# Kernel tuning notes

Hardware: AMD Instinct MI355X
Metric: run time of the kernel (lower is better)

The kernel has to match this reference:

```python
import jax, jax.numpy as jnp
import numpy as np

N_NODES = 50000


def gcn_conv(x, src, dst, W, b, n_nodes):
    """PyG-style GCNConv: x' = D^-1/2 (A + I) D^-1/2 (x W) + b.
    src/dst already include self-loops."""
    h = x @ W  # [N, C_out]
    # symmetric normalization from degree (with self-loops, unit edge weight)
    deg = jax.ops.segment_sum(jnp.ones_like(dst, dtype=h.dtype), dst,
                              num_segments=n_nodes)  # [N]
    dinv = jnp.where(deg > 0, jax.lax.rsqrt(deg), 0.0)
    norm = dinv[src] * dinv[dst]  # [E]
    msg = h[src] * norm[:, None]  # gather + scale, [E, C_out]
    out = jax.ops.segment_sum(msg, dst, num_segments=n_nodes)  # scatter-add
    return out + b


def setup_inputs() -> dict:
    key = jax.random.key(0)
    k1, k2, k3, k4, k5, k6 = jax.random.split(key, 6)
    in_c, hid_c, out_c = 128, 64, 64
    x = jax.random.normal(k1, (N_NODES, in_c), dtype=jnp.float32)
    edge_index = jax.random.randint(k2, (2, 800000), 0, N_NODES, dtype=jnp.int64)
    # Glorot-ish init for weights, zeros for bias (as PyG default)
    W1 = jax.random.normal(k3, (in_c, hid_c), dtype=jnp.float32) / np.sqrt(in_c)
    b1 = jnp.zeros((hid_c,), dtype=jnp.float32)
    W2 = jax.random.normal(k4, (hid_c, out_c), dtype=jnp.float32) / np.sqrt(hid_c)
    b2 = jnp.zeros((out_c,), dtype=jnp.float32)
    return {"x": x, "edge_index": edge_index, "W1": W1, "b1": b1,
            "W2": W2, "b2": b2}


def reference(x, edge_index, W1, b1, W2, b2):
    n = x.shape[0]
    loops = jnp.arange(n, dtype=edge_index.dtype)
    src = jnp.concatenate([edge_index[0], loops])  # add self-loops
    dst = jnp.concatenate([edge_index[1], loops])
    h = gcn_conv(x, src, dst, W1, b1, n)
    h = jax.nn.relu(h)
    return gcn_conv(h, src, dst, W2, b2, n)
```

## Files before the change

kernel.cpp:

```cpp
#include <hip/hip_runtime.h>
#include <hip/hip_fp16.h>


#define C_HID 64

static inline size_t alignup(size_t x) { return (x + 255) & ~(size_t)255; }

typedef __attribute__((address_space(3))) unsigned int lds_uint;
typedef __attribute__((address_space(1))) const unsigned int glob_uint;

__device__ __forceinline__ int blockScanIncl256(int v, int* wsum) {
    const int lane = threadIdx.x & 63, wav = threadIdx.x >> 6;
    int s = v;
#pragma unroll
    for (int off = 1; off < 64; off <<= 1) {
        int t = __shfl_up(s, off);
        if (lane >= off) s += t;
    }
    if (lane == 63) wsum[wav] = s;
    __syncthreads();
    if (wav == 0 && lane < 4) {
        int ws = wsum[lane];
#pragma unroll
        for (int off = 1; off < 4; off <<= 1) {
            int t = __shfl_up(ws, off);
            if (lane >= off) ws += t;
        }
        wsum[lane] = ws;
    }
    __syncthreads();
    return (wav ? wsum[wav - 1] : 0) + s;
}

__device__ __forceinline__ void gridbar(int* bar, int k, int nblk) {
    __syncthreads();
    if (threadIdx.x == 0) {
        __threadfence();
        __hip_atomic_fetch_add(&bar[k], 1, __ATOMIC_RELEASE, __HIP_MEMORY_SCOPE_AGENT);
        while (__hip_atomic_load(&bar[k], __ATOMIC_RELAXED, __HIP_MEMORY_SCOPE_AGENT) < nblk)
            __builtin_amdgcn_s_sleep(2);
        __threadfence();
    }
    __syncthreads();
}

template <int K>
__global__ __launch_bounds__(256) void gemm1_hist_kernel(
    const float* __restrict__ X, const float* __restrict__ W,
    const int* __restrict__ dst, __half* __restrict__ outh,
    int* __restrict__ S, int* __restrict__ bar,
    int n, int E, int ePer, int nb) {
    constexpr int KP = K + 4;
    __shared__ float Xs[64 * KP];
    __shared__ float Ws[K * 64];
    __shared__ int h[256];
    const int t = threadIdx.x;
    const int lane = t & 63;
    const int wav = t >> 6;

    if ((int)blockIdx.x < nb) {
        if (blockIdx.x == 0 && t < 8) bar[t] = 0;
        h[t] = 0;
        __syncthreads();
        int beg = blockIdx.x * ePer, end = min(E, beg + ePer);
        for (int e = beg + t; e < end; e += 256)
            atomicAdd(&h[dst[e] >> 8], 1);
        __syncthreads();
        for (int b = t; b < nb; b += 256)
            S[(size_t)b * nb + blockIdx.x] = h[b];
        return;
    }

    const int row0 = ((int)blockIdx.x - nb) * 64;
    {
        const char* gb = (const char*)W;
        char* lb = (char*)Ws;
        for (int off = wav * 1024; off < K * 64 * 4; off += 4096)
            __builtin_amdgcn_global_load_lds((glob_uint*)(gb + off + lane * 16),
                                             (lds_uint*)(lb + off), 16, 0, 0);
    }
    if (row0 + 64 <= n) {
        const float4* g4 = (const float4*)(X + (size_t)row0 * K);
        for (int i = t; i < 64 * (K / 4); i += 256) {
            float4 v = g4[i];
            int r = i / (K / 4), k0 = (i % (K / 4)) * 4;
            *(float4*)&Xs[r * KP + k0] = v;
        }
    } else {
        for (int i = t; i < 64 * K; i += 256) {
            int r = i / K, k = i % K;
            Xs[r * KP + k] = (row0 + r < n) ? X[(size_t)(row0 + r) * K + k] : 0.0f;
        }
    }
    __syncthreads();

    const int tx = t & 15;
    const int ty = t >> 4;
    float acc[4][4] = {{0.f}};
#pragma unroll 2
    for (int k0 = 0; k0 < K; k0 += 4) {
        float4 a0 = *(const float4*)&Xs[(4 * ty + 0) * KP + k0];
        float4 a1 = *(const float4*)&Xs[(4 * ty + 1) * KP + k0];
        float4 a2 = *(const float4*)&Xs[(4 * ty + 2) * KP + k0];
        float4 a3 = *(const float4*)&Xs[(4 * ty + 3) * KP + k0];
        float4 b0 = *(const float4*)&Ws[(k0 + 0) * 64 + 4 * tx];
        float4 b1 = *(const float4*)&Ws[(k0 + 1) * 64 + 4 * tx];
        float4 b2 = *(const float4*)&Ws[(k0 + 2) * 64 + 4 * tx];
        float4 b3 = *(const float4*)&Ws[(k0 + 3) * 64 + 4 * tx];
        const float* ap[4] = {(const float*)&a0, (const float*)&a1,
                              (const float*)&a2, (const float*)&a3};
        const float* bp[4] = {(const float*)&b0, (const float*)&b1,
                              (const float*)&b2, (const float*)&b3};
#pragma unroll
        for (int r = 0; r < 4; ++r)
#pragma unroll
            for (int kk = 0; kk < 4; ++kk) {
                float av = ap[r][kk];
#pragma unroll
                for (int c = 0; c < 4; ++c)
                    acc[r][c] = fmaf(av, bp[kk][c], acc[r][c]);
            }
    }
#pragma unroll
    for (int r = 0; r < 4; ++r) {
        int row = row0 + 4 * ty + r;
        if (row < n) {
            __half2 p01 = __floats2half2_rn(acc[r][0], acc[r][1]);
            __half2 p23 = __floats2half2_rn(acc[r][2], acc[r][3]);
            float2 st;
            ((__half2*)&st)[0] = p01;
            ((__half2*)&st)[1] = p23;
            *(float2*)&outh[(size_t)row * 64 + 4 * tx] = st;
        }
    }
}

__global__ __launch_bounds__(256) void csr_kernel(
    const int* __restrict__ src, const int* __restrict__ dst, int E, int ePer,
    int* __restrict__ S, int* __restrict__ T, int* __restrict__ bar,
    unsigned* __restrict__ ebuf, int* __restrict__ row_ptr,
    float* __restrict__ dinv, int* __restrict__ esrc, int n, int nb) {
    __shared__ int arr[256];
    __shared__ int texcl[256];
    __shared__ int wsum[4];
    const int b = blockIdx.x;
    const int t = threadIdx.x;

    {
        int v = (t < nb) ? S[(size_t)b * nb + t] : 0;
        int incl = blockScanIncl256(v, wsum);
        if (t < nb) S[(size_t)b * nb + t] = incl - v;
        if (t == 0) T[b] = wsum[3];
    }
    gridbar(bar, 0, nb);

    {
        int v = (t < nb) ? T[t] : 0;
        int incl = blockScanIncl256(v, wsum);
        texcl[t] = incl - v;
    }
    __syncthreads();

    if (t < nb) arr[t] = S[(size_t)t * nb + b] + texcl[t];
    __syncthreads();
    {
        int beg = b * ePer, end = min(E, beg + ePer);
        for (int e = beg + t; e < end; e += 256) {
            int d = dst[e];
            int s = src[e];
            int pos = atomicAdd(&arr[d >> 8], 1);
            ebuf[pos] = ((unsigned)s << 8) | (unsigned)(d & 255);
        }
    }
    gridbar(bar, 1, nb);

    const int node0 = b << 8;
    const int ebeg = texcl[b];
    const int eend = (b + 1 < nb) ? texcl[b + 1] : E;
    arr[t] = 0;
    __syncthreads();
    for (int e = ebeg + t; e < eend; e += 256)
        atomicAdd(&arr[ebuf[e] & 255], 1);
    __syncthreads();
    int deg = arr[t];
    int incl = blockScanIncl256(deg, wsum);
    int excl = incl - deg;
    __syncthreads();
    arr[t] = ebeg + excl;
    int v = node0 + t;
    if (v < n) {
        row_ptr[v + 1] = ebeg + incl;
        dinv[v] = rsqrtf(1.0f + (float)deg);
        if (v == 0) row_ptr[0] = 0;
    }
    __syncthreads();
    for (int e = ebeg + t; e < eend; e += 256) {
        unsigned p = ebuf[e];
        int pos = atomicAdd(&arr[p & 255], 1);
        esrc[pos] = (int)(p >> 8);
    }
}

__global__ __launch_bounds__(256) void agg1_gemm2_kernel(
    const __half* __restrict__ g1, const int* __restrict__ row_ptr,
    const int* __restrict__ esrc, const float* __restrict__ dinv,
    const float* __restrict__ b1, const float* __restrict__ W2,
    __half* __restrict__ g2, int n) {
    __shared__ float Bt[64][68];
    __shared__ float Ws2[64 * 64];
    const int t = threadIdx.x, lane = t & 63, wav = t >> 6;

    {
        const char* gb = (const char*)W2;
        char* lb = (char*)Ws2;
        for (int off = wav * 1024; off < 64 * 64 * 4; off += 4096)
            __builtin_amdgcn_global_load_lds((glob_uint*)(gb + off + lane * 16),
                                             (lds_uint*)(lb + off), 16, 0, 0);
    }

    const int g = t >> 2;
    const int c = t & 3;
    const int row0 = blockIdx.x * 64;
    const int v = row0 + g;
    const float4* __restrict__ hs4 = (const float4*)g1;

    if (v < n) {
        float acc[16];
        float dv0 = dinv[v];
        {
            size_t rb = (size_t)v * 8 + 2 * c;
            float4 r0 = hs4[rb], r1 = hs4[rb + 1];
            const __half2* h0 = (const __half2*)&r0;
            const __half2* h1 = (const __half2*)&r1;
#pragma unroll
            for (int q = 0; q < 4; ++q) {
                float2 f0 = __half22float2(h0[q]);
                float2 f1 = __half22float2(h1[q]);
                acc[2 * q] = f0.x * dv0;     acc[2 * q + 1] = f0.y * dv0;
                acc[8 + 2 * q] = f1.x * dv0; acc[9 + 2 * q] = f1.y * dv0;
            }
        }
        const int beg = row_ptr[v], end = row_ptr[v + 1];
        int j = beg;
        for (; j + 2 <= end; j += 2) {
            int s0 = esrc[j], s1 = esrc[j + 1];
            float d0 = dinv[s0], d1 = dinv[s1];
            size_t rb0 = (size_t)s0 * 8 + 2 * c, rb1 = (size_t)s1 * 8 + 2 * c;
            float4 a0 = hs4[rb0], a1 = hs4[rb0 + 1];
            float4 e0 = hs4[rb1], e1 = hs4[rb1 + 1];
            const __half2* pa0 = (const __half2*)&a0;
            const __half2* pa1 = (const __half2*)&a1;
            const __half2* pe0 = (const __half2*)&e0;
            const __half2* pe1 = (const __half2*)&e1;
#pragma unroll
            for (int q = 0; q < 4; ++q) {
                float2 f;
                f = __half22float2(pa0[q]);
                acc[2 * q] = fmaf(f.x, d0, acc[2 * q]);
                acc[2 * q + 1] = fmaf(f.y, d0, acc[2 * q + 1]);
                f = __half22float2(pa1[q]);
                acc[8 + 2 * q] = fmaf(f.x, d0, acc[8 + 2 * q]);
                acc[9 + 2 * q] = fmaf(f.y, d0, acc[9 + 2 * q]);
                f = __half22float2(pe0[q]);
                acc[2 * q] = fmaf(f.x, d1, acc[2 * q]);
                acc[2 * q + 1] = fmaf(f.y, d1, acc[2 * q + 1]);
                f = __half22float2(pe1[q]);
                acc[8 + 2 * q] = fmaf(f.x, d1, acc[8 + 2 * q]);
                acc[9 + 2 * q] = fmaf(f.y, d1, acc[9 + 2 * q]);
            }
        }
        if (j < end) {
            int s0 = esrc[j];
            float d0 = dinv[s0];
            size_t rb0 = (size_t)s0 * 8 + 2 * c;
            float4 a0 = hs4[rb0], a1 = hs4[rb0 + 1];
            const __half2* pa0 = (const __half2*)&a0;
            const __half2* pa1 = (const __half2*)&a1;
#pragma unroll
            for (int q = 0; q < 4; ++q) {
                float2 f;
                f = __half22float2(pa0[q]);
                acc[2 * q] = fmaf(f.x, d0, acc[2 * q]);
                acc[2 * q + 1] = fmaf(f.y, d0, acc[2 * q + 1]);
                f = __half22float2(pa1[q]);
                acc[8 + 2 * q] = fmaf(f.x, d0, acc[8 + 2 * q]);
                acc[9 + 2 * q] = fmaf(f.y, d0, acc[9 + 2 * q]);
            }
        }
        const float* bb = b1 + c * 16;
#pragma unroll
        for (int u = 0; u < 4; ++u) {
            float4 w;
            w.x = fmaxf(fmaf(acc[4 * u + 0], dv0, bb[4 * u + 0]), 0.f);
            w.y = fmaxf(fmaf(acc[4 * u + 1], dv0, bb[4 * u + 1]), 0.f);
            w.z = fmaxf(fmaf(acc[4 * u + 2], dv0, bb[4 * u + 2]), 0.f);
            w.w = fmaxf(fmaf(acc[4 * u + 3], dv0, bb[4 * u + 3]), 0.f);
            *(float4*)&Bt[g][c * 16 + 4 * u] = w;
        }
    } else {
#pragma unroll
        for (int u = 0; u < 4; ++u)
            *(float4*)&Bt[g][c * 16 + 4 * u] = make_float4(0.f, 0.f, 0.f, 0.f);
    }
    __syncthreads();

    const int tx = t & 15;
    const int ty = t >> 4;
    float a2[4][4] = {{0.f}};
#pragma unroll 2
    for (int k0 = 0; k0 < 64; k0 += 4) {
        float4 x0 = *(const float4*)&Bt[4 * ty + 0][k0];
        float4 x1 = *(const float4*)&Bt[4 * ty + 1][k0];
        float4 x2 = *(const float4*)&Bt[4 * ty + 2][k0];
        float4 x3 = *(const float4*)&Bt[4 * ty + 3][k0];
        float4 w0 = *(const float4*)&Ws2[(k0 + 0) * 64 + 4 * tx];
        float4 w1 = *(const float4*)&Ws2[(k0 + 1) * 64 + 4 * tx];
        float4 w2 = *(const float4*)&Ws2[(k0 + 2) * 64 + 4 * tx];
        float4 w3 = *(const float4*)&Ws2[(k0 + 3) * 64 + 4 * tx];
        const float* xp[4] = {(const float*)&x0, (const float*)&x1,
                              (const float*)&x2, (const float*)&x3};
        const float* wp[4] = {(const float*)&w0, (const float*)&w1,
                              (const float*)&w2, (const float*)&w3};
#pragma unroll
        for (int r = 0; r < 4; ++r)
#pragma unroll
            for (int kk = 0; kk < 4; ++kk) {
                float av = xp[r][kk];
#pragma unroll
                for (int cc = 0; cc < 4; ++cc)
                    a2[r][cc] = fmaf(av, wp[kk][cc], a2[r][cc]);
            }
    }
#pragma unroll
    for (int r = 0; r < 4; ++r) {
        int row = row0 + 4 * ty + r;
        if (row < n) {
            float dv = dinv[row];
            __half2 p01 = __floats2half2_rn(a2[r][0] * dv, a2[r][1] * dv);
            __half2 p23 = __floats2half2_rn(a2[r][2] * dv, a2[r][3] * dv);
            float2 st;
            ((__half2*)&st)[0] = p01;
            ((__half2*)&st)[1] = p23;
            *(float2*)&g2[(size_t)row * 64 + 4 * tx] = st;
        }
    }
}

__global__ __launch_bounds__(256) void aggregate2_kernel(
    const __half* __restrict__ hs,
    const int* __restrict__ row_ptr,
    const int* __restrict__ esrc,
    const float* __restrict__ dinv,
    const float* __restrict__ bias,
    float* __restrict__ out, int n) {
    const int v = blockIdx.x * 32 + (threadIdx.x >> 3);
    if (v >= n) return;
    const int c8 = threadIdx.x & 7;
    const float4* __restrict__ hs4 = (const float4*)hs;

    const int beg = row_ptr[v];
    const int end = row_ptr[v + 1];

    float acc[8];
    {
        float4 raw = hs4[(size_t)v * 8 + c8];
        const __half2* hp = (const __half2*)&raw;
#pragma unroll
        for (int q = 0; q < 4; ++q) {
            float2 f = __half22float2(hp[q]);
            acc[2 * q] = f.x; acc[2 * q + 1] = f.y;
        }
    }

    int j = beg;
    for (; j + 4 <= end; j += 4) {
        int s0 = esrc[j], s1 = esrc[j + 1], s2 = esrc[j + 2], s3 = esrc[j + 3];
        float4 r0 = hs4[(size_t)s0 * 8 + c8];
        float4 r1 = hs4[(size_t)s1 * 8 + c8];
        float4 r2 = hs4[(size_t)s2 * 8 + c8];
        float4 r3 = hs4[(size_t)s3 * 8 + c8];
        const __half2* h0 = (const __half2*)&r0;
        const __half2* h1 = (const __half2*)&r1;
        const __half2* h2 = (const __half2*)&r2;
        const __half2* h3 = (const __half2*)&r3;
#pragma unroll
        for (int q = 0; q < 4; ++q) {
            float2 f0 = __half22float2(h0[q]);
            float2 f1 = __half22float2(h1[q]);
            float2 f2 = __half22float2(h2[q]);
            float2 f3 = __half22float2(h3[q]);
            acc[2 * q]     += (f0.x + f1.x) + (f2.x + f3.x);
            acc[2 * q + 1] += (f0.y + f1.y) + (f2.y + f3.y);
        }
    }
    for (; j < end; ++j) {
        int s0 = esrc[j];
        float4 r0 = hs4[(size_t)s0 * 8 + c8];
        const __half2* h0 = (const __half2*)&r0;
#pragma unroll
        for (int q = 0; q < 4; ++q) {
            float2 f0 = __half22float2(h0[q]);
            acc[2 * q] += f0.x;
            acc[2 * q + 1] += f0.y;
        }
    }

    float dv = dinv[v];
    float4 b0 = *(const float4*)(bias + c8 * 8);
    float4 b1v = *(const float4*)(bias + c8 * 8 + 4);
    float4 o0, o1;
    o0.x = fmaf(acc[0], dv, b0.x); o0.y = fmaf(acc[1], dv, b0.y);
    o0.z = fmaf(acc[2], dv, b0.z); o0.w = fmaf(acc[3], dv, b0.w);
    o1.x = fmaf(acc[4], dv, b1v.x); o1.y = fmaf(acc[5], dv, b1v.y);
    o1.z = fmaf(acc[6], dv, b1v.z); o1.w = fmaf(acc[7], dv, b1v.w);
    float4* op = (float4*)(out + (size_t)v * 64 + c8 * 8);
    op[0] = o0;
    op[1] = o1;
}

extern "C" void kernel_launch(void* const* d_in, const int* in_sizes, int n_in,
                              void* d_out, int out_size, void* d_ws, size_t ws_size,
                              hipStream_t stream) {
    const float* x  = (const float*)d_in[0];
    const int*   ei = (const int*)d_in[1];
    const float* W1 = (const float*)d_in[2];
    const float* b1 = (const float*)d_in[3];
    const float* W2 = (const float*)d_in[4];
    const float* b2 = (const float*)d_in[5];
    float* out = (float*)d_out;

    const int C_IN = 128;
    const int n = in_sizes[0] / C_IN;
    const int E = in_sizes[1] / 2;
    const int* src = ei;
    const int* dst = ei + E;

    const int nb = (n + 255) >> 8;
    const int ngb = (n + 63) / 64;
    const int ePer = (E + nb - 1) / nb;

    char* w = (char*)d_ws;
    float*    dinv    = (float*)w;    w += alignup((size_t)n * sizeof(float));
    __half*   g1      = (__half*)w;   w += alignup((size_t)n * C_HID * sizeof(__half));
    __half*   g2      = (__half*)w;   w += alignup((size_t)n * C_HID * sizeof(__half));
    int*      row_ptr = (int*)w;      w += alignup((size_t)(n + 1) * sizeof(int));
    int*      S       = (int*)w;      w += alignup(((size_t)nb * nb + nb) * sizeof(int));
    int*      T       = S + (size_t)nb * nb;
    int*      bar     = (int*)w;      w += alignup(64 * sizeof(int));
    unsigned* ebuf    = (unsigned*)w; w += alignup((size_t)E * sizeof(unsigned));
    int*      esrc    = (int*)w;

    gemm1_hist_kernel<128><<<nb + ngb, 256, 0, stream>>>(
        x, W1, dst, g1, S, bar, n, E, ePer, nb);

    csr_kernel<<<nb, 256, 0, stream>>>(
        src, dst, E, ePer, S, T, bar, ebuf, row_ptr, dinv, esrc, n, nb);

    agg1_gemm2_kernel<<<ngb, 256, 0, stream>>>(
        g1, row_ptr, esrc, dinv, b1, W2, g2, n);

    aggregate2_kernel<<<(n + 31) / 32, 256, 0, stream>>>(
        g2, row_ptr, esrc, dinv, b2, out, n);
}
```

Before: 192.3 us.

## Replace grid-barrier CSR kernel with separate scan, scatter and build kernels

Splits the single persistent CSR-construction kernel, which used two software grid barriers built on atomics and spin-waits, into four kernels: per-row scan, scan of block totals, edge scatter, and per-bucket row-pointer build. Kernel boundaries now provide the ordering, which removes the barrier spinning and the need to reset barrier counters. The cost is three extra kernel launches, and the tiny single-block scan kernel adds serial latency between stages.

```diff
diff --git a/kernel.cpp b/kernel.cpp
--- a/kernel.cpp
+++ b/kernel.cpp
@@ -30,26 +30,13 @@
     }
     __syncthreads();
     return (wav ? wsum[wav - 1] : 0) + s;
-}
-
-__device__ __forceinline__ void gridbar(int* bar, int k, int nblk) {
-    __syncthreads();
-    if (threadIdx.x == 0) {
-        __threadfence();
-        __hip_atomic_fetch_add(&bar[k], 1, __ATOMIC_RELEASE, __HIP_MEMORY_SCOPE_AGENT);
-        while (__hip_atomic_load(&bar[k], __ATOMIC_RELAXED, __HIP_MEMORY_SCOPE_AGENT) < nblk)
-            __builtin_amdgcn_s_sleep(2);
-        __threadfence();
-    }
-    __syncthreads();
 }
 
 template <int K>
 __global__ __launch_bounds__(256) void gemm1_hist_kernel(
     const float* __restrict__ X, const float* __restrict__ W,
     const int* __restrict__ dst, __half* __restrict__ outh,
-    int* __restrict__ S, int* __restrict__ bar,
-    int n, int E, int ePer, int nb) {
+    int* __restrict__ S, int n, int E, int ePer, int nb) {
     constexpr int KP = K + 4;
     __shared__ float Xs[64 * KP];
     __shared__ float Ws[K * 64];
@@ -59,7 +46,6 @@
     const int wav = t >> 6;
 
     if ((int)blockIdx.x < nb) {
-        if (blockIdx.x == 0 && t < 8) bar[t] = 0;
         h[t] = 0;
         __syncthreads();
         int beg = blockIdx.x * ePer, end = min(E, beg + ePer);
@@ -135,48 +121,53 @@
     }
 }
 
-__global__ __launch_bounds__(256) void csr_kernel(
+__global__ __launch_bounds__(256) void scan_rows_kernel(
+    int* __restrict__ S, int* __restrict__ T, int nb) {
+    __shared__ int wsum[4];
+    const int b = blockIdx.x, t = threadIdx.x;
+    int v = (t < nb) ? S[(size_t)b * nb + t] : 0;
+    int incl = blockScanIncl256(v, wsum);
+    if (t < nb) S[(size_t)b * nb + t] = incl - v;
+    if (t == 0) T[b] = wsum[3];
+}
+
+__global__ __launch_bounds__(256) void scan_T_kernel(int* __restrict__ T, int nb) {
+    __shared__ int wsum[4];
+    const int t = threadIdx.x;
+    int v = (t < nb) ? T[t] : 0;
+    int incl = blockScanIncl256(v, wsum);
+    if (t < nb) T[t] = incl - v;
+    if (t == nb - 1) T[nb] = incl;
+}
+
+__global__ __launch_bounds__(256) void scatter_kernel(
     const int* __restrict__ src, const int* __restrict__ dst, int E, int ePer,
-    int* __restrict__ S, int* __restrict__ T, int* __restrict__ bar,
-    unsigned* __restrict__ ebuf, int* __restrict__ row_ptr,
-    float* __restrict__ dinv, int* __restrict__ esrc, int n, int nb) {
+    const int* __restrict__ S, const int* __restrict__ T,
+    unsigned* __restrict__ ebuf, int nb) {
     __shared__ int arr[256];
-    __shared__ int texcl[256];
+    const int b = blockIdx.x, t = threadIdx.x;
+    if (t < nb) arr[t] = S[(size_t)t * nb + b] + T[t];
+    __syncthreads();
+    int beg = b * ePer, end = min(E, beg + ePer);
+    for (int e = beg + t; e < end; e += 256) {
+        int d = dst[e];
+        int s = src[e];
+        int pos = atomicAdd(&arr[d >> 8], 1);
+        ebuf[pos] = ((unsigned)s << 8) | (unsigned)(d & 255);
+    }
+}
+
+__global__ __launch_bounds__(256) void build_kernel(
+    const unsigned* __restrict__ ebuf, const int* __restrict__ T,
+    int* __restrict__ row_ptr, float* __restrict__ dinv,
+    int* __restrict__ esrc, int n, int nb) {
+    __shared__ int arr[256];
     __shared__ int wsum[4];
-    const int b = blockIdx.x;
-    const int t = threadIdx.x;
-
-    {
-        int v = (t < nb) ? S[(size_t)b * nb + t] : 0;
-        int incl = blockScanIncl256(v, wsum);
-        if (t < nb) S[(size_t)b * nb + t] = incl - v;
-        if (t == 0) T[b] = wsum[3];
-    }
-    gridbar(bar, 0, nb);
-
-    {
-        int v = (t < nb) ? T[t] : 0;
-        int incl = blockScanIncl256(v, wsum);
-        texcl[t] = incl - v;
-    }
-    __syncthreads();
-
-    if (t < nb) arr[t] = S[(size_t)t * nb + b] + texcl[t];
-    __syncthreads();
-    {
-        int beg = b * ePer, end = min(E, beg + ePer);
-        for (int e = beg + t; e < end; e += 256) {
-            int d = dst[e];
-            int s = src[e];
-            int pos = atomicAdd(&arr[d >> 8], 1);
-            ebuf[pos] = ((unsigned)s << 8) | (unsigned)(d & 255);
-        }
-    }
-    gridbar(bar, 1, nb);
-
+    const int b = blockIdx.x, t = threadIdx.x;
     const int node0 = b << 8;
-    const int ebeg = texcl[b];
-    const int eend = (b + 1 < nb) ? texcl[b + 1] : E;
+    const int ebeg = T[b];
+    const int eend = T[b + 1];
+
     arr[t] = 0;
     __syncthreads();
     for (int e = ebeg + t; e < eend; e += 256)
@@ -444,17 +435,18 @@
     __half*   g1      = (__half*)w;   w += alignup((size_t)n * C_HID * sizeof(__half));
     __half*   g2      = (__half*)w;   w += alignup((size_t)n * C_HID * sizeof(__half));
     int*      row_ptr = (int*)w;      w += alignup((size_t)(n + 1) * sizeof(int));
-    int*      S       = (int*)w;      w += alignup(((size_t)nb * nb + nb) * sizeof(int));
-    int*      T       = S + (size_t)nb * nb;
-    int*      bar     = (int*)w;      w += alignup(64 * sizeof(int));
+    int*      S       = (int*)w;      w += alignup((size_t)nb * nb * sizeof(int));
+    int*      T       = (int*)w;      w += alignup((size_t)(nb + 1) * sizeof(int));
     unsigned* ebuf    = (unsigned*)w; w += alignup((size_t)E * sizeof(unsigned));
     int*      esrc    = (int*)w;
 
     gemm1_hist_kernel<128><<<nb + ngb, 256, 0, stream>>>(
-        x, W1, dst, g1, S, bar, n, E, ePer, nb);
-
-    csr_kernel<<<nb, 256, 0, stream>>>(
-        src, dst, E, ePer, S, T, bar, ebuf, row_ptr, dinv, esrc, n, nb);
+        x, W1, dst, g1, S, n, E, ePer, nb);
+
+    scan_rows_kernel<<<nb, 256, 0, stream>>>(S, T, nb);
+    scan_T_kernel<<<1, 256, 0, stream>>>(T, nb);
+    scatter_kernel<<<nb, 256, 0, stream>>>(src, dst, E, ePer, S, T, ebuf, nb);
+    build_kernel<<<nb, 256, 0, stream>>>(ebuf, T, row_ptr, dinv, esrc, n, nb);
 
     agg1_gemm2_kernel<<<ngb, 256, 0, stream>>>(
         g1, row_ptr, esrc, dinv, b1, W2, g2, n);
```

After: 162.4 us. 1.18x faster.
